# Optimization experiments

Hardware: AMD Instinct MI355X
Metric: run time of the kernel (lower is better)

Reference implementation:

```python
import jax, jax.numpy as jnp
import numpy as np

B, N, C, H, NL, NH = 8, 1024, 256, 512, 3, 8


def setup_inputs() -> dict:
    key = jax.random.key(0)
    ks = jax.random.split(key, 16)
    g = lambda k, shape: jax.random.normal(k, shape, jnp.float32) * 0.02
    return dict(
        concept_features=jax.random.normal(ks[0], (B, N, C), jnp.float32),
        adjacency_matrix=jax.random.uniform(ks[1], (B, N, N), jnp.float32),
        edge_types=jax.random.randint(ks[2], (B, N, N), 0, 10),
        concept_mask=jnp.ones((B, N), bool),
        W_emb=g(ks[3], (H, C)), b_emb=jnp.zeros((H,), jnp.float32),
        W_in=g(ks[4], (NL, 3 * H, H)), b_in=jnp.zeros((NL, 3 * H), jnp.float32),
        W_out=g(ks[5], (NL, H, H)), b_out=jnp.zeros((NL, H), jnp.float32),
        W_conv=g(ks[6], (NL, H, H)), b_conv=jnp.zeros((NL, H), jnp.float32),
        W_cls=g(ks[7], (1, H)), b_cls=jnp.zeros((1,), jnp.float32),
        W_diff=g(ks[8], (5, H)), b_diff=jnp.zeros((5,), jnp.float32),
        W_pre=g(ks[9], (1, 2 * H)), b_pre=jnp.zeros((1,), jnp.float32),
        W_pool=g(ks[10], (H, H)), b_pool=jnp.zeros((H,), jnp.float32),
    )


def reference(concept_features, adjacency_matrix, edge_types, concept_mask,
              W_emb, b_emb, W_in, b_in, W_out, b_out, W_conv, b_conv,
              W_cls, b_cls, W_diff, b_diff, W_pre, b_pre, W_pool, b_pool):
    Bq, Nc, _ = concept_features.shape
    Hd = W_emb.shape[0]
    dh = Hd // NH

    def mha(x, Wi, bi, Wo, bo):
        # torch nn.MultiheadAttention with batch_first=False: the (B,N,H)
        # input is treated as (seq=B, batch=N, embed=H) -> attention over B.
        qkv = x @ Wi.T + bi                      # (B,N,3H)
        q, k, v = jnp.split(qkv, 3, axis=-1)
        rs = lambda t: t.reshape(Bq, Nc, NH, dh)
        q, k, v = rs(q), rs(k), rs(v)
        sc = jnp.einsum('inhd,jnhd->nhij', q, k) / jnp.sqrt(jnp.float32(dh))
        a = jax.nn.softmax(sc, axis=-1)          # (N,NH,B,B)
        o = jnp.einsum('nhij,jnhd->inhd', a, v).reshape(Bq, Nc, Hd)
        return o @ Wo.T + bo

    def ln(x):  # F.layer_norm, no affine
        m = x.mean(-1, keepdims=True)
        v = ((x - m) ** 2).mean(-1, keepdims=True)
        return (x - m) * jax.lax.rsqrt(v + 1e-5)

    x = concept_features @ W_emb.T + b_emb       # (B,N,H)
    for l in range(W_in.shape[0]):
        att = mha(x, W_in[l], b_in[l], W_out[l], b_out[l])
        conv = att @ W_conv[l].T + b_conv[l]
        agg = jnp.einsum('bij,bjh->bih', adjacency_matrix, conv)
        x = ln(x + agg)

    mastery = x @ W_cls.T + b_cls                # (B,N,1)
    diff = x @ W_diff.T + b_diff                 # (B,N,5)

    # O(N^2) pairwise loop -> bilinear decomposition:
    # score(i,j) = x_i @ W_pre[:, :H].T + x_j @ W_pre[:, H:].T + b
    h1 = (x @ W_pre[:, :Hd].T)[..., 0]           # (B,N)
    h2 = (x @ W_pre[:, Hd:].T)[..., 0]           # (B,N)
    pair = h1[:, :, None] + h2[:, None, :] + b_pre[0]  # (B,N,N)
    off = ~np.eye(Nc, dtype=bool).reshape(-1)    # static mask, i!=j row-major
    prereq = pair.reshape(Bq, Nc * Nc)[:, off][..., None]  # (B,N*(N-1),1)

    graph = x.mean(axis=1) @ W_pool.T + b_pool   # (B,H)
    return (x, mastery, diff, prereq, graph)
```

## Files before the change

kernel.cpp:

```cpp
#include <hip/hip_runtime.h>
#include <hip/hip_bf16.h>

typedef unsigned short ushort_t;
typedef __attribute__((ext_vector_type(4))) float floatx4;
typedef __attribute__((ext_vector_type(8))) __bf16 bf16x8;
typedef __attribute__((ext_vector_type(4))) unsigned short ushortx4;
typedef __attribute__((ext_vector_type(8))) unsigned short ushortx8;

static __device__ __forceinline__ float b2f(ushort_t u) {
  union { unsigned int i; float f; } v; v.i = ((unsigned int)u) << 16; return v.f;
}
static __device__ __forceinline__ ushort_t f2b(float f) {
  unsigned int x = __float_as_uint(f);
  unsigned int r = (x + 0x7fffu + ((x >> 16) & 1u)) >> 16;
  return (ushort_t)r;
}
static __device__ __forceinline__ void glds16(const ushort_t* g, ushort_t* l) {
  __builtin_amdgcn_global_load_lds(
      (const __attribute__((address_space(1))) unsigned int*)g,
      (__attribute__((address_space(3))) unsigned int*)l, 16, 0, 0);
}

template<int MODE>
static __device__ __forceinline__ void gemm_core(
    const ushort_t* __restrict__ Ab, const ushort_t* __restrict__ Bm,
    const float* __restrict__ bias,
    ushort_t* __restrict__ outB, ushort_t* __restrict__ C1,
    int N, int K, int m0, int n0, int kbeg, int kend,
    ushort_t* As, ushort_t* Bs)
{
  const int tid  = threadIdx.x;
  const int wid  = tid >> 6;
  const int lane = tid & 63;
  const int quad = lane >> 4;
  const int l16  = lane & 15;

  const int wr = (wid >> 1) * 64;
  const int wc = (wid & 1) * 64;

  const int srow = tid >> 3;
  const int scj  = ((tid & 7) ^ (srow & 7)) * 8;
  const long abase = (long)(m0 + srow) * K + scj;
  const long bbase = (long)(n0 + srow) * K + scj;

  floatx4 acc[4][4];
#pragma unroll
  for (int i = 0; i < 4; ++i)
#pragma unroll
    for (int j = 0; j < 4; ++j) acc[i][j] = (floatx4){0.f, 0.f, 0.f, 0.f};

  const int rx = l16 & 7;

  for (int k0 = kbeg; k0 < kend; k0 += 64) {
    __syncthreads();
#pragma unroll
    for (int p = 0; p < 4; ++p)
      glds16(Ab + abase + 32 * p * (long)K + k0, &As[tid * 8 + p * 2048]);
#pragma unroll
    for (int p = 0; p < 4; ++p)
      glds16(Bm + bbase + 32 * p * (long)K + k0, &Bs[tid * 8 + p * 2048]);
    __syncthreads();

#pragma unroll
    for (int kk = 0; kk < 2; ++kk) {
      bf16x8 a[4], b[4];
#pragma unroll
      for (int i = 0; i < 4; ++i)
        a[i] = *(const bf16x8*)(&As[(wr + i * 16 + l16) * 64 +
                                    (((kk * 4 + quad) ^ rx) << 3)]);
#pragma unroll
      for (int j = 0; j < 4; ++j)
        b[j] = *(const bf16x8*)(&Bs[(wc + j * 16 + l16) * 64 +
                                    (((kk * 4 + quad) ^ rx) << 3)]);
#pragma unroll
      for (int i = 0; i < 4; ++i)
#pragma unroll
        for (int j = 0; j < 4; ++j)
          acc[i][j] = __builtin_amdgcn_mfma_f32_16x16x32_bf16(a[i], b[j], acc[i][j], 0, 0, 0);
    }
  }

#pragma unroll
  for (int j = 0; j < 4; ++j) {
    int col = n0 + wc + j * 16 + l16;
    float bv = (bias != nullptr) ? bias[col] : 0.f;
#pragma unroll
    for (int i = 0; i < 4; ++i) {
      int mbase = m0 + wr + i * 16 + quad * 4;
      if constexpr (MODE == 1) {
#pragma unroll
        for (int r = 0; r < 4; ++r)
          outB[(long)(mbase + r) * N + col] = f2b(acc[i][j][r] + bv);
      } else if constexpr (MODE == 2) {
        int b = mbase >> 10, jrow = mbase & 1023;
        ushortx4 pk;
#pragma unroll
        for (int r = 0; r < 4; ++r) pk[r] = f2b(acc[i][j][r] + bv);
        *(ushortx4*)(outB + ((long)b * N + col) * 1024 + jrow) = pk;
      } else {
        ushort_t* o = (n0 < 512) ? outB : C1;
        const int cw = (n0 < 512) ? 512 : 1536;
        const int cc = (n0 < 512) ? col : col - 512;
#pragma unroll
        for (int r = 0; r < 4; ++r)
          o[(long)(mbase + r) * cw + cc] = f2b(acc[i][j][r] + bv);
      }
    }
  }
}

template<int MODE, int KS>
__global__ __launch_bounds__(256, 3) void gemm_bt(
    const ushort_t* __restrict__ Ab, const ushort_t* __restrict__ Bm,
    const float* __restrict__ bias,
    ushort_t* __restrict__ C0, ushort_t* __restrict__ C1,
    int N, int K, long aBatch, long bBatch, long cBatch)
{
  __shared__ __align__(16) ushort_t As[128 * 64];
  __shared__ __align__(16) ushort_t Bs[128 * 64];
  const int lin = blockIdx.y * gridDim.x + blockIdx.x;
  const int m0 = (lin % gridDim.y) * 128;
  const int n0 = (lin / gridDim.y) * 128;
  const int z  = (KS > 1) ? (int)(blockIdx.z / KS) : blockIdx.z;
  const int kq = (KS > 1) ? (int)(blockIdx.z % KS) : 0;
  const int kbeg = kq * (K / KS);
  const int kend = kbeg + (K / KS);
  ushort_t* outB = (KS >= 2 && kq == 1) ? C1 : C0;
  gemm_core<MODE>(Ab + (long)z * aBatch, Bm + (long)z * bBatch, bias,
                  outB + ((MODE == 1) ? (long)z * cBatch : 0), C1,
                  N, K, m0, n0, kbeg, kend, As, Bs);
}

__global__ __launch_bounds__(256, 3) void setup_gemm(
    const ushort_t* __restrict__ Wcb, const ushort_t* __restrict__ WoT,
    ushort_t* __restrict__ Wfb,
    const ushort_t* __restrict__ Winb, const ushort_t* __restrict__ WembT,
    ushort_t* __restrict__ Wq0t)
{
  __shared__ __align__(16) ushort_t As[128 * 64];
  __shared__ __align__(16) ushort_t Bs[128 * 64];
  const int lin = blockIdx.x;
  const int z = blockIdx.z;
  if (z < 3) {
    if (lin >= 16) return;
    const long off = (long)z * 262144;
    gemm_core<1>(Wcb + off, WoT + off, nullptr, Wfb + off, nullptr,
                 512, 512, (lin & 3) * 128, (lin >> 2) * 128, 0, 512, As, Bs);
  } else {
    gemm_core<1>(Winb, WembT, nullptr, Wq0t, nullptr,
                 256, 512, (lin % 12) * 128, (lin / 12) * 128, 0, 512, As, Bs);
  }
}

__global__ __launch_bounds__(256) void prep_kernel(
    const float* __restrict__ Win,  ushort_t* __restrict__ Winb,
    const float* __restrict__ Wemb, ushort_t* __restrict__ Wq0,
    const float* __restrict__ Wconv, ushort_t* __restrict__ Wcb,
    const float* __restrict__ ADJ,  ushort_t* __restrict__ ADJb,
    const float* __restrict__ CF,   ushort_t* __restrict__ CFb,
    const float* __restrict__ Wout, ushort_t* __restrict__ WoT,
    const float* __restrict__ bout, const float* __restrict__ bconv,
    float* __restrict__ bfused,
    ushort_t* __restrict__ WembT,
    const float* __restrict__ bemb, const float* __restrict__ bin0,
    float* __restrict__ bcat)
{
  __shared__ float tile[64][65];
  const int bid = blockIdx.x, tid = threadIdx.x;
  if (bid < 6720) {
    const float* src; ushort_t* dst; long i;
    if (bid < 1152)      { src = Win;   dst = Winb; i = (long)bid * 256 + tid; }
    else if (bid < 1216) { src = Wemb;  dst = Wq0;  i = (long)(bid - 1152) * 256 + tid; }
    else if (bid < 1600) { src = Wconv; dst = Wcb;  i = (long)(bid - 1216) * 256 + tid; }
    else if (bid < 5696) { src = ADJ;   dst = ADJb; i = (long)(bid - 1600) * 256 + tid; }
    else                 { src = CF;    dst = CFb;  i = (long)(bid - 5696) * 256 + tid; }
    floatx4 a = ((const floatx4*)src)[2 * i];
    floatx4 b = ((const floatx4*)src)[2 * i + 1];
    ushortx4 ha, hb;
#pragma unroll
    for (int r = 0; r < 4; ++r) { ha[r] = f2b(a[r]); hb[r] = f2b(b[r]); }
    ((ushortx4*)dst)[2 * i] = ha; ((ushortx4*)dst)[2 * i + 1] = hb;
  } else if (bid < 6912) {
    const int t = bid - 6720;
    const int z = t >> 6, k0 = ((t >> 3) & 7) * 64, j0 = (t & 7) * 64;
    const long base = (long)z * 262144;
#pragma unroll
    for (int p = 0; p < 16; ++p) {
      int idx = tid + p * 256;
      int jj = idx >> 6, kk = idx & 63;
      tile[jj][kk] = Wout[base + (long)(j0 + jj) * 512 + k0 + kk];
    }
    __syncthreads();
#pragma unroll
    for (int p = 0; p < 16; ++p) {
      int idx = tid + p * 256;
      int kk = idx >> 6, jj = idx & 63;
      WoT[base + (long)(k0 + kk) * 512 + j0 + jj] = f2b(tile[jj][kk]);
    }
  } else if (bid < 6944) {
    const int t = bid - 6912;
    const int j0 = (t >> 2) * 64, k0 = (t & 3) * 64;
#pragma unroll
    for (int p = 0; p < 16; ++p) {
      int idx = tid + p * 256;
      int jj = idx >> 6, kk = idx & 63;
      tile[jj][kk] = Wemb[(long)(j0 + jj) * 256 + k0 + kk];
    }
    __syncthreads();
#pragma unroll
    for (int p = 0; p < 16; ++p) {
      int idx = tid + p * 256;
      int kk = idx >> 6, jj = idx & 63;
      WembT[(long)(k0 + kk) * 512 + j0 + jj] = f2b(tile[jj][kk]);
    }
  } else if (bid < 7328) {
    const int w = tid >> 6, lane = tid & 63;
    const int gi = (bid - 6944) * 4 + w;
    const int l = gi >> 9, o = gi & 511;
    float p = 0.f;
#pragma unroll
    for (int k = 0; k < 8; ++k)
      p += Wconv[(long)l * 262144 + (long)o * 512 + lane + 64 * k] *
           bout[l * 512 + lane + 64 * k];
#pragma unroll
    for (int msk = 1; msk <= 32; msk <<= 1) p += __shfl_xor(p, msk);
    if (lane == 0) bfused[gi] = p + bconv[l * 512 + o];
  } else if (bid < 7712) {
    const int w = tid >> 6, lane = tid & 63;
    const int o = (bid - 7328) * 4 + w;
    float p = 0.f;
#pragma unroll
    for (int k = 0; k < 8; ++k)
      p += Win[(long)o * 512 + lane + 64 * k] * bemb[lane + 64 * k];
#pragma unroll
    for (int msk = 1; msk <= 32; msk <<= 1) p += __shfl_xor(p, msk);
    if (lane == 0) bcat[512 + o] = p + bin0[o];
  } else {
    int idx = (bid - 7712) * 256 + tid;
    bcat[idx] = bemb[idx];
  }
}

__global__ __launch_bounds__(512, 8) void attn_kernel(
    const ushort_t* __restrict__ qkv, ushort_t* __restrict__ outp)
{
  __shared__ ushort_t qs[8 * 1544];
  __shared__ float aw[8][64];
  const int tid = threadIdx.x;
  const int n = blockIdx.x;

  const ushort_t* src = qkv + (long)n * 1536;
#pragma unroll
  for (int p = 0; p < 3; ++p) {
    int c = tid + p * 512;
    int i = c / 192, off = (c % 192) * 8;
    *(ushortx8*)(&qs[i * 1544 + off]) =
        *(const ushortx8*)(src + (long)i * 1024 * 1536 + off);
  }
  __syncthreads();

  const int h    = tid >> 6;
  const int lane = tid & 63;
  const int i = lane >> 3, j = lane & 7;
  const ushort_t* qrow = &qs[i * 1544 + h * 64];
  const ushort_t* krow = &qs[j * 1544 + 512 + h * 64];
  float s = 0.f;
#pragma unroll
  for (int c8 = 0; c8 < 8; ++c8) {
    ushortx8 qa = *(const ushortx8*)(qrow + c8 * 8);
    ushortx8 ka = *(const ushortx8*)(krow + c8 * 8);
#pragma unroll
    for (int r = 0; r < 8; ++r) s += b2f(qa[r]) * b2f(ka[r]);
  }
  s *= 0.125f;

  float m = s;
  m = fmaxf(m, __shfl_xor(m, 1));
  m = fmaxf(m, __shfl_xor(m, 2));
  m = fmaxf(m, __shfl_xor(m, 4));
  float e = __expf(s - m);
  float sum = e;
  sum += __shfl_xor(sum, 1);
  sum += __shfl_xor(sum, 2);
  sum += __shfl_xor(sum, 4);
  aw[h][lane] = e / sum;

  float vv[8];
#pragma unroll
  for (int jj = 0; jj < 8; ++jj)
    vv[jj] = b2f(qs[jj * 1544 + 1024 + h * 64 + lane]);
  const long ob = (long)n * 512 + h * 64 + lane;
#pragma unroll
  for (int ii = 0; ii < 8; ++ii) {
    float acc = 0.f;
#pragma unroll
    for (int jj = 0; jj < 8; ++jj) acc += aw[h][ii * 8 + jj] * vv[jj];
    outp[ob + (long)ii * 1024 * 512] = f2b(acc);
  }
}

__global__ __launch_bounds__(256) void ln_kernel(
    const ushort_t* __restrict__ xb,
    const ushort_t* __restrict__ aggA, const ushort_t* __restrict__ aggB,
    ushort_t* __restrict__ outB)
{
  const int w = threadIdx.x >> 6, lane = threadIdx.x & 63;
  const long base = ((long)blockIdx.x * 4 + w) * 512;
  float v[8];
  float s = 0.f;
#pragma unroll
  for (int k = 0; k < 8; ++k) {
    long idx = base + lane + 64 * k;
    v[k] = b2f(xb[idx]) + b2f(aggA[idx]) + b2f(aggB[idx]);
    s += v[k];
  }
#pragma unroll
  for (int msk = 1; msk <= 32; msk <<= 1) s += __shfl_xor(s, msk);
  float mean = s * (1.f / 512.f);
  float vv = 0.f;
#pragma unroll
  for (int k = 0; k < 8; ++k) { float d = v[k] - mean; vv += d * d; }
#pragma unroll
  for (int msk = 1; msk <= 32; msk <<= 1) vv += __shfl_xor(vv, msk);
  float inv = rsqrtf(vv * (1.f / 512.f) + 1e-5f);
#pragma unroll
  for (int k = 0; k < 8; ++k)
    outB[base + lane + 64 * k] = f2b((v[k] - mean) * inv);
}

__global__ __launch_bounds__(256) void final_ln_heads_kernel(
    const ushort_t* __restrict__ xb,
    const ushort_t* __restrict__ aggA, const ushort_t* __restrict__ aggB,
    float* __restrict__ out_x,
    const float* __restrict__ Wcls, const float* __restrict__ bcls,
    const float* __restrict__ Wdiff, const float* __restrict__ bdiff,
    const float* __restrict__ Wpre,
    float* __restrict__ mastery, float* __restrict__ diff,
    float* __restrict__ h1, float* __restrict__ h2,
    float* __restrict__ xp)
{
  __shared__ float sp4[4][512];
  const int w = threadIdx.x >> 6, lane = threadIdx.x & 63;
  const long row = (long)blockIdx.x * 4 + w;
  const long base = row * 512;
  float v[8];
  float s = 0.f;
#pragma unroll
  for (int k = 0; k < 8; ++k) {
    long idx = base + lane + 64 * k;
    v[k] = b2f(xb[idx]) + b2f(aggA[idx]) + b2f(aggB[idx]);
    s += v[k];
  }
#pragma unroll
  for (int msk = 1; msk <= 32; msk <<= 1) s += __shfl_xor(s, msk);
  float mean = s * (1.f / 512.f);
  float vv = 0.f;
#pragma unroll
  for (int k = 0; k < 8; ++k) { float d = v[k] - mean; vv += d * d; }
#pragma unroll
  for (int msk = 1; msk <= 32; msk <<= 1) vv += __shfl_xor(vv, msk);
  float inv = rsqrtf(vv * (1.f / 512.f) + 1e-5f);
#pragma unroll
  for (int k = 0; k < 8; ++k) {
    v[k] = (v[k] - mean) * inv;
    out_x[base + lane + 64 * k] = v[k];
    sp4[w][lane + 64 * k] = v[k];
  }
  __syncthreads();
  for (int t = threadIdx.x; t < 512; t += 256)
    xp[(long)blockIdx.x * 512 + t] =
        sp4[0][t] + sp4[1][t] + sp4[2][t] + sp4[3][t];
#pragma unroll
  for (int o = 0; o < 8; ++o) {
    const float* wp = (o == 0) ? Wcls
                    : (o <= 5) ? (Wdiff + (o - 1) * 512)
                    : (o == 6) ? Wpre : (Wpre + 512);
    float p = 0.f;
#pragma unroll
    for (int k = 0; k < 8; ++k) p += v[k] * wp[lane + 64 * k];
#pragma unroll
    for (int msk = 1; msk <= 32; msk <<= 1) p += __shfl_xor(p, msk);
    if (lane == 0) {
      if (o == 0)      mastery[row] = p + bcls[0];
      else if (o <= 5) diff[row * 5 + (o - 1)] = p + bdiff[o - 1];
      else if (o == 6) h1[row] = p;
      else             h2[row] = p;
    }
  }
}

__global__ __launch_bounds__(256) void epi_kernel(
    const float* __restrict__ h1, const float* __restrict__ h2,
    const float* __restrict__ bpre, float* __restrict__ outp,
    const float* __restrict__ xp, const float* __restrict__ Wpool,
    const float* __restrict__ bpool, float* __restrict__ g)
{
  __shared__ float xms[512];
  const int bid = blockIdx.x;
  if (bid < 2048) {
#pragma unroll
    for (int rr = 0; rr < 4; ++rr) {
      const int ri = bid * 4 + rr;
      const int b = ri >> 10, i = ri & 1023;
      const float base = h1[ri] + bpre[0];
      const long ob = (long)b * (1024 * 1023) + (long)i * 1023;
      const float* h2b = h2 + b * 1024;
#pragma unroll
      for (int r = 0; r < 4; ++r) {
        int j = r * 256 + threadIdx.x;
        if (j == i) continue;
        int pos = (j < i) ? j : j - 1;
        outp[ob + pos] = base + h2b[j];
      }
    }
  } else {
    const int b = bid - 2048;
    const float* p = xp + (long)b * 256 * 512;
#pragma unroll
    for (int cc = 0; cc < 2; ++cc) {
      int c = threadIdx.x + cc * 256;
      float s = 0.f;
      for (int q = 0; q < 256; ++q) s += p[q * 512 + c];
      xms[c] = s;
    }
    __syncthreads();
#pragma unroll
    for (int oo = 0; oo < 2; ++oo) {
      int o = threadIdx.x + oo * 256;
      const float* wr = Wpool + (long)o * 512;
      float s = 0.f;
      for (int hh = 0; hh < 512; ++hh) s += xms[hh] * wr[hh];
      g[b * 512 + o] = s * (1.f / 1024.f) + bpool[o];
    }
  }
}

extern "C" void kernel_launch(void* const* d_in, const int* in_sizes, int n_in,
                              void* d_out, int out_size, void* d_ws, size_t ws_size,
                              hipStream_t stream)
{
  const float* CF    = (const float*)d_in[0];
  const float* ADJ   = (const float*)d_in[1];
  const float* Wemb  = (const float*)d_in[4];
  const float* bemb  = (const float*)d_in[5];
  const float* Win   = (const float*)d_in[6];
  const float* bin   = (const float*)d_in[7];
  const float* Wout  = (const float*)d_in[8];
  const float* bout  = (const float*)d_in[9];
  const float* Wconv = (const float*)d_in[10];
  const float* bconv = (const float*)d_in[11];
  const float* Wcls  = (const float*)d_in[12];
  const float* bcls  = (const float*)d_in[13];
  const float* Wdiff = (const float*)d_in[14];
  const float* bdiff = (const float*)d_in[15];
  const float* Wpre  = (const float*)d_in[16];
  const float* bpre  = (const float*)d_in[17];
  const float* Wpool = (const float*)d_in[18];
  const float* bpool = (const float*)d_in[19];

  ushort_t* W = (ushort_t*)d_ws;
  ushort_t* xb   = W;
  ushort_t* qkvb = W + 4194304;
  ushort_t* cT    = qkvb;
  ushort_t* aggA  = qkvb + 4194304;
  ushort_t* aggB  = qkvb + 8388608;
  ushort_t* WoT   = qkvb + 4194304;
  ushort_t* Wcb   = qkvb + 4980736;
  ushort_t* WembT = qkvb + 5767168;
  ushort_t* Winb = W + 16777216;
  ushort_t* Wfb  = W + 19136512;
  ushort_t* ADJb = W + 19922944;
  ushort_t* CFb  = W + 28311552;
  ushort_t* Wq0  = W + 32505856;
  float* bfused = (float*)(W + 33030144);
  float* bcat   = bfused + 1536;
  float* h1     = bcat + 2048;
  float* h2     = h1 + 8192;
  float* xp     = h2 + 8192;

  float* out_x       = (float*)d_out;
  float* out_mastery = out_x + 4194304;
  float* out_diff    = out_mastery + 8192;
  float* out_prereq  = out_diff + 40960;
  float* out_graph   = out_prereq + 8380416;
  ushort_t* aob = (ushort_t*)out_x;

  dim3 blk(256);

  prep_kernel<<<dim3(7714), blk, 0, stream>>>(
      Win, Winb, Wemb, Wq0, Wconv, Wcb, ADJ, ADJb, CF, CFb,
      Wout, WoT, bout, bconv, bfused, WembT, bemb, bin, bcat);
  setup_gemm<<<dim3(24, 1, 4), blk, 0, stream>>>(
      Wcb, WoT, Wfb, Winb, WembT, Wq0 + 512 * 256);

  for (int l = 0; l < 3; ++l) {
    if (l == 0) {
      gemm_bt<3, 1><<<dim3(16, 64, 1), blk, 0, stream>>>(
          CFb, Wq0, bcat, xb, qkvb, 2048, 256, 0, 0, 0);
    } else {
      gemm_bt<1, 1><<<dim3(12, 64, 1), blk, 0, stream>>>(
          xb, Winb + (long)l * 786432, bin + l * 1536,
          qkvb, nullptr, 1536, 512, 0, 0, 0);
    }
    attn_kernel<<<dim3(1024), dim3(512), 0, stream>>>(qkvb, aob);
    gemm_bt<2, 1><<<dim3(4, 64, 1), blk, 0, stream>>>(
        aob, Wfb + (long)l * 262144, bfused + l * 512,
        cT, nullptr, 512, 512, 0, 0, 0);
    gemm_bt<1, 2><<<dim3(4, 8, 16), blk, 0, stream>>>(
        ADJb, cT, nullptr, aggA, aggB,
        512, 1024, 1048576, 524288, 524288);
    if (l < 2)
      ln_kernel<<<dim3(2048), blk, 0, stream>>>(xb, aggA, aggB, xb);
    else
      final_ln_heads_kernel<<<dim3(2048), blk, 0, stream>>>(
          xb, aggA, aggB, out_x, Wcls, bcls, Wdiff, bdiff, Wpre,
          out_mastery, out_diff, h1, h2, xp);
  }

  epi_kernel<<<dim3(2056), blk, 0, stream>>>(h1, h2, bpre, out_prereq,
                                             xp, Wpool, bpool, out_graph);
}
```

Measured before the change: 432.9 us.

## Vectorize prereq writes and split graph pooling into parallel partial sums

The pairwise prereq output is now written as contiguous float4 stores over the flattened output, with (i,j) recovered by division, instead of scattered scalar writes per row. The graph-pool tail is split: the epilogue computes 32-row partial column sums across 64 blocks, and a new small kernel reduces them and applies a transposed Wpool (transposed once in prep) for coalesced weight reads. This removes the serial 256-row sums in 8 blocks and the uncoalesced Wpool row reads, at the cost of an extra kernel launch, extra workspace and integer divides per element.

```diff
diff --git a/kernel.cpp b/kernel.cpp
--- a/kernel.cpp
+++ b/kernel.cpp
@@ -163,7 +163,8 @@
     float* __restrict__ bfused,
     ushort_t* __restrict__ WembT,
     const float* __restrict__ bemb, const float* __restrict__ bin0,
-    float* __restrict__ bcat)
+    float* __restrict__ bcat,
+    const float* __restrict__ Wpool, float* __restrict__ WpT)
 {
   __shared__ float tile[64][65];
   const int bid = blockIdx.x, tid = threadIdx.x;
@@ -235,9 +236,25 @@
 #pragma unroll
     for (int msk = 1; msk <= 32; msk <<= 1) p += __shfl_xor(p, msk);
     if (lane == 0) bcat[512 + o] = p + bin0[o];
-  } else {
+  } else if (bid < 7714) {
     int idx = (bid - 7712) * 256 + tid;
     bcat[idx] = bemb[idx];
+  } else {
+    const int t = bid - 7714;
+    const int j0 = (t >> 3) * 64, k0 = (t & 7) * 64;
+#pragma unroll
+    for (int p = 0; p < 16; ++p) {
+      int idx = tid + p * 256;
+      int jj = idx >> 6, kk = idx & 63;
+      tile[jj][kk] = Wpool[(long)(j0 + jj) * 512 + k0 + kk];
+    }
+    __syncthreads();
+#pragma unroll
+    for (int p = 0; p < 16; ++p) {
+      int idx = tid + p * 256;
+      int kk = idx >> 6, jj = idx & 63;
+      WpT[(long)(k0 + kk) * 512 + j0 + jj] = tile[jj][kk];
+    }
   }
 }
 
@@ -392,46 +409,63 @@
 __global__ __launch_bounds__(256) void epi_kernel(
     const float* __restrict__ h1, const float* __restrict__ h2,
     const float* __restrict__ bpre, float* __restrict__ outp,
-    const float* __restrict__ xp, const float* __restrict__ Wpool,
-    const float* __restrict__ bpool, float* __restrict__ g)
-{
-  __shared__ float xms[512];
+    const float* __restrict__ xp, float* __restrict__ xq)
+{
   const int bid = blockIdx.x;
-  if (bid < 2048) {
-#pragma unroll
-    for (int rr = 0; rr < 4; ++rr) {
-      const int ri = bid * 4 + rr;
-      const int b = ri >> 10, i = ri & 1023;
-      const float base = h1[ri] + bpre[0];
-      const long ob = (long)b * (1024 * 1023) + (long)i * 1023;
-      const float* h2b = h2 + b * 1024;
-#pragma unroll
-      for (int r = 0; r < 4; ++r) {
-        int j = r * 256 + threadIdx.x;
-        if (j == i) continue;
-        int pos = (j < i) ? j : j - 1;
-        outp[ob + pos] = base + h2b[j];
-      }
-    }
+  if (bid < 8184) {
+    const int g = bid * 256 + threadIdx.x;
+    const int t = g * 4;
+    const int b = t / 1047552;
+    const int r = t - b * 1047552;
+    const float bp = bpre[0];
+    const float* h1b = h1 + b * 1024;
+    const float* h2b = h2 + b * 1024;
+    floatx4 o;
+#pragma unroll
+    for (int k = 0; k < 4; ++k) {
+      int rk = r + k;
+      int i = rk / 1023;
+      int pos = rk - i * 1023;
+      int j = pos + (pos >= i);
+      o[k] = h1b[i] + bp + h2b[j];
+    }
+    *(floatx4*)(outp + t) = o;
   } else {
-    const int b = bid - 2048;
-    const float* p = xp + (long)b * 256 * 512;
+    const int q0 = bid - 8184;
+    const float* p = xp + (long)q0 * 32 * 512;
 #pragma unroll
     for (int cc = 0; cc < 2; ++cc) {
       int c = threadIdx.x + cc * 256;
       float s = 0.f;
-      for (int q = 0; q < 256; ++q) s += p[q * 512 + c];
-      xms[c] = s;
-    }
-    __syncthreads();
-#pragma unroll
-    for (int oo = 0; oo < 2; ++oo) {
-      int o = threadIdx.x + oo * 256;
-      const float* wr = Wpool + (long)o * 512;
-      float s = 0.f;
-      for (int hh = 0; hh < 512; ++hh) s += xms[hh] * wr[hh];
-      g[b * 512 + o] = s * (1.f / 1024.f) + bpool[o];
-    }
+#pragma unroll
+      for (int q = 0; q < 32; ++q) s += p[q * 512 + c];
+      xq[(long)q0 * 512 + c] = s;
+    }
+  }
+}
+
+__global__ __launch_bounds__(256) void graph_kernel(
+    const float* __restrict__ xq, const float* __restrict__ WpT,
+    const float* __restrict__ bpool, float* __restrict__ g)
+{
+  __shared__ float xms[512];
+  const int b = blockIdx.x;
+  const float* xb = xq + (long)b * 8 * 512;
+#pragma unroll
+  for (int cc = 0; cc < 2; ++cc) {
+    int c = threadIdx.x + cc * 256;
+    float s = 0.f;
+#pragma unroll
+    for (int p = 0; p < 8; ++p) s += xb[p * 512 + c];
+    xms[c] = s;
+  }
+  __syncthreads();
+#pragma unroll
+  for (int oo = 0; oo < 2; ++oo) {
+    int o = threadIdx.x + oo * 256;
+    float acc = 0.f;
+    for (int h = 0; h < 512; ++h) acc += xms[h] * WpT[h * 512 + o];
+    g[b * 512 + o] = acc * (1.f / 1024.f) + bpool[o];
   }
 }
 
@@ -477,6 +511,8 @@
   float* h1     = bcat + 2048;
   float* h2     = h1 + 8192;
   float* xp     = h2 + 8192;
+  float* xq     = xp + 1048576;
+  float* WpT    = xq + 32768;
 
   float* out_x       = (float*)d_out;
   float* out_mastery = out_x + 4194304;
@@ -487,9 +523,10 @@
 
   dim3 blk(256);
 
-  prep_kernel<<<dim3(7714), blk, 0, stream>>>(
+  prep_kernel<<<dim3(7778), blk, 0, stream>>>(
       Win, Winb, Wemb, Wq0, Wconv, Wcb, ADJ, ADJb, CF, CFb,
-      Wout, WoT, bout, bconv, bfused, WembT, bemb, bin, bcat);
+      Wout, WoT, bout, bconv, bfused, WembT, bemb, bin, bcat,
+      Wpool, WpT);
   setup_gemm<<<dim3(24, 1, 4), blk, 0, stream>>>(
       Wcb, WoT, Wfb, Winb, WembT, Wq0 + 512 * 256);
 
@@ -517,6 +554,7 @@
           out_mastery, out_diff, h1, h2, xp);
   }
 
-  epi_kernel<<<dim3(2056), blk, 0, stream>>>(h1, h2, bpre, out_prereq,
-                                             xp, Wpool, bpool, out_graph);
-}
+  epi_kernel<<<dim3(8248), blk, 0, stream>>>(h1, h2, bpre, out_prereq,
+                                             xp, xq);
+  graph_kernel<<<dim3(8), blk, 0, stream>>>(xq, WpT, bpool, out_graph);
+}
```

Result: faster. 423.3 us (-2.2%).
